# Kernel optimization log

Hardware: AMD Instinct MI355X
Metric: run time of the kernel (lower is better)

Reference implementation:

```python
import jax, jax.numpy as jnp
import numpy as np

B, S, H, NH = 2, 2048, 2048, 16
HD = H // NH  # 128


def setup_inputs() -> dict:
    key = jax.random.key(0)
    ks = jax.random.split(key, 10)
    scale = 0.02
    hidden_states = jax.random.normal(ks[0], (B, S, H), dtype=jnp.float32)
    # additive causal mask [1,1,S,S]
    causal = jnp.tril(jnp.ones((S, S), dtype=jnp.bool_))
    attention_mask = jnp.where(causal, 0.0, -1e9).astype(jnp.float32)[None, None]
    def lin(k):
        kw, kb = jax.random.split(k)
        return (jax.random.normal(kw, (H, H), dtype=jnp.float32) * scale,
                jnp.zeros((H,), dtype=jnp.float32))
    Wq, bq = lin(ks[1])
    Wk, bk = lin(ks[2])
    Wv, bv = lin(ks[3])
    Wo, bo = lin(ks[4])
    return {"hidden_states": hidden_states, "attention_mask": attention_mask,
            "Wq": Wq, "bq": bq, "Wk": Wk, "bk": bk, "Wv": Wv, "bv": bv,
            "Wo": Wo, "bo": bo}


def reference(hidden_states, attention_mask, Wq, bq, Wk, bk, Wv, bv, Wo, bo):
    b, s, h = hidden_states.shape
    def shape(t):  # [b,s,h] -> [b,nh,s,hd]
        return t.reshape(b, s, NH, HD).transpose(0, 2, 1, 3)
    q = shape(hidden_states @ Wq.T + bq)
    k = shape(hidden_states @ Wk.T + bk)
    v = shape(hidden_states @ Wv.T + bv)
    attn = jnp.einsum('bnqd,bnkd->bnqk', q, k) / jnp.sqrt(jnp.float32(HD))
    attn = attn + attention_mask
    attn = jax.nn.softmax(attn, axis=-1)
    out = jnp.einsum('bnqk,bnkd->bnqd', attn, v)
    out = out.transpose(0, 2, 1, 3).reshape(b, s, h)
    return out @ Wo.T + bo
```

## Files before the change

kernel.cpp:

```cpp
#include <hip/hip_runtime.h>
#include <hip/hip_bf16.h>

#define SEQ   2048
#define HDIM  2048
#define NHEAD 16
#define HEADD 128
#define BATCH 2
#define MTOT  (BATCH*SEQ)
#define BH    (BATCH*NHEAD)

typedef __attribute__((ext_vector_type(8))) __bf16 bf16x8;
typedef __attribute__((ext_vector_type(4))) float f32x4;
typedef __attribute__((ext_vector_type(16))) float f32x16;
typedef __attribute__((ext_vector_type(8))) unsigned short u16x8;

__device__ __forceinline__ unsigned short f2b(float f) {
    __bf16 h = (__bf16)f;
    return __builtin_bit_cast(unsigned short, h);
}

__device__ __forceinline__ void gld_lds16(const void* gptr, void* ldsptr) {
    __builtin_amdgcn_global_load_lds(
        (const __attribute__((address_space(1))) unsigned int*)gptr,
        (__attribute__((address_space(3))) unsigned int*)ldsptr,
        16, 0, 0);
}

__global__ void cvt_bf16(const float* __restrict__ src, unsigned short* __restrict__ dst, long n8) {
    long i = blockIdx.x * (long)blockDim.x + threadIdx.x;
    long stride = (long)gridDim.x * blockDim.x;
    for (; i < n8; i += stride) {
        f32x4 a = *(const f32x4*)(src + i * 8);
        f32x4 b = *(const f32x4*)(src + i * 8 + 4);
        u16x8 o;
#pragma unroll
        for (int j = 0; j < 4; ++j) { o[j] = f2b(a[j]); o[4 + j] = f2b(b[j]); }
        *(u16x8*)(dst + i * 8) = o;
    }
}

__global__ void cvt5(const float* __restrict__ s0, const float* __restrict__ s1,
                     const float* __restrict__ s2, const float* __restrict__ s3,
                     const float* __restrict__ s4,
                     unsigned short* __restrict__ d0, unsigned short* __restrict__ d1,
                     unsigned short* __restrict__ d2, unsigned short* __restrict__ d3,
                     unsigned short* __restrict__ d4,
                     long n0, long n1) {
    const float* s; unsigned short* d; long n;
    switch (blockIdx.z) {
        case 0: s = s0; d = d0; n = n0; break;
        case 1: s = s1; d = d1; n = n1; break;
        case 2: s = s2; d = d2; n = n1; break;
        case 3: s = s3; d = d3; n = n1; break;
        default: s = s4; d = d4; n = n1; break;
    }
    long i = blockIdx.x * (long)blockDim.x + threadIdx.x;
    long stride = (long)gridDim.x * blockDim.x;
    for (; i < n; i += stride) {
        f32x4 a = *(const f32x4*)(s + i * 8);
        f32x4 b = *(const f32x4*)(s + i * 8 + 4);
        u16x8 o;
#pragma unroll
        for (int j = 0; j < 4; ++j) { o[j] = f2b(a[j]); o[4 + j] = f2b(b[j]); }
        *(u16x8*)(d + i * 8) = o;
    }
}

__launch_bounds__(256)
__global__ void gemm_qkv(const unsigned short* __restrict__ A,
                         const unsigned short* __restrict__ Bw,
                         const float* __restrict__ bq, const float* __restrict__ bk,
                         const float* __restrict__ bv,
                         unsigned short* __restrict__ Cout, float rs) {
    __shared__ unsigned short As[128 * 32];
    __shared__ unsigned short Bs[128 * 32];
    const int tid  = threadIdx.x;
    const int lane = tid & 63;
    const int w    = tid >> 6;

    const int wgid = blockIdx.y * gridDim.x + blockIdx.x;
    const int cpx  = (gridDim.x * gridDim.y) >> 3;
    const int swz  = (wgid & 7) * cpx + (wgid >> 3);
    const int m0  = (swz % gridDim.x) * 128;
    const int n0g = (swz / gridDim.x) * 128;

    const int wr = (w >> 1) * 64, wc = (w & 1) * 64;
    const long rowBytes = (long)HDIM * 2;

    const char* Ab = (const char*)A  + (long)m0  * rowBytes;
    const char* Bb = (const char*)Bw + (long)n0g * rowBytes;

    f32x4 acc[4][4] = {};

    const int kIters = HDIM >> 5;
    for (int kt = 0; kt < kIters; ++kt) {
        const long kb = (long)kt * 64;
#pragma unroll
        for (int i = 0; i < 2; ++i) {
            int c = tid + i * 256;
            int row = c >> 2;
            int cb  = (c & 3) * 16;
            gld_lds16(Ab + (long)row * rowBytes + kb + cb, (char*)As + c * 16);
            gld_lds16(Bb + (long)row * rowBytes + kb + cb, (char*)Bs + c * 16);
        }
        __syncthreads();
        bf16x8 af[4], bfr[4];
#pragma unroll
        for (int f = 0; f < 4; ++f) {
            af[f]  = *(const bf16x8*)&As[(wr + f * 16 + (lane & 15)) * 32 + (lane >> 4) * 8];
            bfr[f] = *(const bf16x8*)&Bs[(wc + f * 16 + (lane & 15)) * 32 + (lane >> 4) * 8];
        }
#pragma unroll
        for (int mf = 0; mf < 4; ++mf)
#pragma unroll
            for (int nf = 0; nf < 4; ++nf)
                acc[mf][nf] = __builtin_amdgcn_mfma_f32_16x16x32_bf16(af[mf], bfr[nf], acc[mf][nf], 0, 0, 0);
        __syncthreads();
    }

    const int mat = n0g >> 11;
    const float* bb = (mat == 0) ? bq : (mat == 1) ? bk : bv;
    const float scale = (mat == 0) ? rs : 1.0f;
    unsigned short* O = Cout + (long)mat * 8388608;

#pragma unroll
    for (int mf = 0; mf < 4; ++mf) {
#pragma unroll
        for (int nf = 0; nf < 4; ++nf) {
            int nn = (n0g + wc + nf * 16 + (lane & 15)) & 2047;
            int nh = nn >> 7, hd = nn & 127;
            float bv_ = bb[nn];
#pragma unroll
            for (int j = 0; j < 4; ++j) {
                int m = m0 + wr + mf * 16 + (lane >> 4) * 4 + j;
                int b = m >> 11, s = m & 2047;
                float v = (acc[mf][nf][j] + bv_) * scale;
                long idx;
                if (mat < 2) idx = ((long)(b * NHEAD + nh) * SEQ + s) * HEADD + hd;
                else         idx = ((long)(b * NHEAD + nh) * HEADD + hd) * SEQ + s;
                O[idx] = f2b(v);
            }
        }
    }
}

__launch_bounds__(256)
__global__ void gemm_out(const unsigned short* __restrict__ A,
                         const unsigned short* __restrict__ Bw,
                         const float* __restrict__ bias,
                         float* __restrict__ Cout) {
    __shared__ unsigned short As[128 * 32];
    __shared__ unsigned short Bs[128 * 32];
    const int tid  = threadIdx.x;
    const int lane = tid & 63;
    const int w    = tid >> 6;

    const int wgid = blockIdx.y * gridDim.x + blockIdx.x;
    const int cpx  = (gridDim.x * gridDim.y) >> 3;
    const int swz  = (wgid & 7) * cpx + (wgid >> 3);
    const int m0 = (swz % gridDim.x) * 128, n0 = (swz / gridDim.x) * 128;

    const int wr = (w >> 1) * 64, wc = (w & 1) * 64;
    const long rowBytes = (long)HDIM * 2;

    f32x4 acc[4][4] = {};

    const int kIters = HDIM >> 5;
    for (int kt = 0; kt < kIters; ++kt) {
        const long kb = (long)kt * 64;
#pragma unroll
        for (int i = 0; i < 2; ++i) {
            int c = tid + i * 256;
            int row = c >> 2;
            int cb  = (c & 3) * 16;
            gld_lds16((const char*)A  + (long)(m0 + row) * rowBytes + kb + cb, (char*)As + c * 16);
            gld_lds16((const char*)Bw + (long)(n0 + row) * rowBytes + kb + cb, (char*)Bs + c * 16);
        }
        __syncthreads();
        bf16x8 af[4], bfr[4];
#pragma unroll
        for (int f = 0; f < 4; ++f) {
            af[f]  = *(const bf16x8*)&As[(wr + f * 16 + (lane & 15)) * 32 + (lane >> 4) * 8];
            bfr[f] = *(const bf16x8*)&Bs[(wc + f * 16 + (lane & 15)) * 32 + (lane >> 4) * 8];
        }
#pragma unroll
        for (int mf = 0; mf < 4; ++mf)
#pragma unroll
            for (int nf = 0; nf < 4; ++nf)
                acc[mf][nf] = __builtin_amdgcn_mfma_f32_16x16x32_bf16(af[mf], bfr[nf], acc[mf][nf], 0, 0, 0);
        __syncthreads();
    }

#pragma unroll
    for (int mf = 0; mf < 4; ++mf) {
#pragma unroll
        for (int nf = 0; nf < 4; ++nf) {
            int n = n0 + wc + nf * 16 + (lane & 15);
            float bv = bias[n];
#pragma unroll
            for (int j = 0; j < 4; ++j) {
                int m = m0 + wr + mf * 16 + (lane >> 4) * 4 + j;
                Cout[(long)m * HDIM + n] = acc[mf][nf][j] + bv;
            }
        }
    }
}

#define MASKV (-3.0e38f)

__device__ __forceinline__ void attn_step32s(
    const unsigned short* Ksb, const unsigned short* Vsb,
    const bf16x8 (&qf)[8], f32x16 (&acc)[4], float& mrun, float& lrun,
    int lane, int p, int q0w, int kvt, bool diag)
{
    const int ql = lane & 31;
    const int hi = lane >> 5;

    f32x16 sv = {};
    {
        const int row = p * 32 + ql;
        const int sw  = (row & 7) << 4;
        __builtin_amdgcn_s_setprio(1);
#pragma unroll
        for (int kc = 0; kc < 8; ++kc) {
            int off = (row * 256 + ((kc * 32 + hi * 16) ^ sw)) >> 1;
            bf16x8 kf = *(const bf16x8*)&Ksb[off];
            sv = __builtin_amdgcn_mfma_f32_32x32x16_bf16(kf, qf[kc], sv, 0, 0, 0);
        }
        __builtin_amdgcn_s_setprio(0);
    }

    if (diag) {
        const int qg = q0w + ql;
#pragma unroll
        for (int r = 0; r < 16; ++r) {
            int kv = kvt * 64 + p * 32 + (r & 3) + 8 * (r >> 2) + 4 * hi;
            if (kv > qg) sv[r] = MASKV;
        }
    }

    float tmax = sv[0];
#pragma unroll
    for (int r = 1; r < 16; ++r) tmax = fmaxf(tmax, sv[r]);
    tmax = fmaxf(tmax, __shfl_xor(tmax, 32));

    float mnew = mrun, sc = 1.0f;
    if (__any(tmax > mrun + 11.5f)) {
        mnew = fmaxf(mrun, tmax);
        sc = exp2f(mrun - mnew);
#pragma unroll
        for (int db = 0; db < 4; ++db) acc[db] *= sc;
    }
    float rsum = 0.f;
#pragma unroll
    for (int r = 0; r < 16; ++r) {
        float pv = exp2f(sv[r] - mnew);
        sv[r] = pv;
        rsum += pv;
    }
    rsum += __shfl_xor(rsum, 32);
    lrun = lrun * sc + rsum;
    mrun = mnew;

    bf16x8 pf[2];
#pragma unroll
    for (int kc2 = 0; kc2 < 2; ++kc2) {
        unsigned int w01 = f2b(sv[8 * kc2 + 0]) | ((unsigned int)f2b(sv[8 * kc2 + 1]) << 16);
        unsigned int w23 = f2b(sv[8 * kc2 + 2]) | ((unsigned int)f2b(sv[8 * kc2 + 3]) << 16);
        unsigned int w45 = f2b(sv[8 * kc2 + 4]) | ((unsigned int)f2b(sv[8 * kc2 + 5]) << 16);
        unsigned int w67 = f2b(sv[8 * kc2 + 6]) | ((unsigned int)f2b(sv[8 * kc2 + 7]) << 16);
        asm volatile("v_permlane32_swap_b32 %0, %1" : "+v"(w01), "+v"(w45));
        asm volatile("v_permlane32_swap_b32 %0, %1" : "+v"(w23), "+v"(w67));
        union { unsigned int u[4]; bf16x8 v; } pk;
        pk.u[0] = w01; pk.u[1] = w23; pk.u[2] = w45; pk.u[3] = w67;
        pf[kc2] = pk.v;
    }

    __builtin_amdgcn_s_setprio(1);
#pragma unroll
    for (int db = 0; db < 4; ++db) {
        const int row = db * 32 + ql;
        const int sw  = (row & 7) << 4;
#pragma unroll
        for (int kc2 = 0; kc2 < 2; ++kc2) {
            int off = (row * 128 + ((p * 64 + kc2 * 32 + hi * 16) ^ sw)) >> 1;
            bf16x8 vf = *(const bf16x8*)&Vsb[off];
            acc[db] = __builtin_amdgcn_mfma_f32_32x32x16_bf16(vf, pf[kc2], acc[db], 0, 0, 0);
        }
    }
    __builtin_amdgcn_s_setprio(0);
}

__device__ __forceinline__ void attn_merge_store(
    f32x16 (&acc)[4], float mrun, float lrun,
    float (*Mx)[32], float (*Lx)[32], f32x16 (*Ob)[64],
    unsigned short* __restrict__ Out, long rowbase, int lane, int wp, int p)
{
    const int ql = lane & 31, hi = lane >> 5;
    Mx[wp * 2 + p][ql] = mrun;
    Lx[wp * 2 + p][ql] = lrun;
    __syncthreads();
    const float mo = Mx[wp * 2 + 1 - p][ql];
    const float lo = Lx[wp * 2 + 1 - p][ql];
    const float M  = fmaxf(mrun, mo);
    const float a  = exp2f(mrun - M);
    const float L  = lrun * a + lo * exp2f(mo - M);
#pragma unroll
    for (int db = 0; db < 4; ++db) acc[db] *= a;
#pragma unroll
    for (int db = 0; db < 4; ++db) {
        if (p == 1) Ob[wp][lane] = acc[db];
        __syncthreads();
        if (p == 0) acc[db] += Ob[wp][lane];
        __syncthreads();
    }
    if (p == 0) {
        const float inv = 1.0f / L;
        const long base = rowbase + (long)ql * HDIM;
#pragma unroll
        for (int db = 0; db < 4; ++db)
#pragma unroll
            for (int mm = 0; mm < 4; ++mm) {
                int d0 = db * 32 + 8 * mm + 4 * hi;
                unsigned int w0 = f2b(acc[db][4 * mm + 0] * inv) | ((unsigned int)f2b(acc[db][4 * mm + 1] * inv) << 16);
                unsigned int w1 = f2b(acc[db][4 * mm + 2] * inv) | ((unsigned int)f2b(acc[db][4 * mm + 3] * inv) << 16);
                *(unsigned long long*)(Out + base + d0) =
                    (unsigned long long)w0 | ((unsigned long long)w1 << 32);
            }
    }
}

__launch_bounds__(512, 1)
__global__ void attn_fwd(const unsigned short* __restrict__ Q,
                         const unsigned short* __restrict__ K,
                         const unsigned short* __restrict__ Vt,
                         unsigned short* __restrict__ Out) {
    __shared__ unsigned short Ks[2][64 * 128];
    __shared__ unsigned short Vs[2][128 * 64];
    __shared__ float Mx[8][32];
    __shared__ float Lx[8][32];
    __shared__ f32x16 Ob[4][64];

    const int tid  = threadIdx.x;
    const int lane = tid & 63;
    const int w    = tid >> 6;
    const int wp   = w & 3;
    const int p    = w >> 2;

    const int id  = blockIdx.x;
    const int xcd = id & 7;
    const int j   = id >> 3;
    const int bh  = xcd * 4 + (j >> 3);
    const int x   = j & 7;
    const int hiT = 15 - x;
    const int loT = x;
    const int nA  = 2 * hiT + 2;
    const int nB  = 2 * loT + 2;
    const int q0A = hiT * 128 + wp * 32;
    const int q0B = loT * 128 + wp * 32;

    const char* Kbase = (const char*)(K  + (long)bh * SEQ * HEADD);
    const char* Vbase = (const char*)(Vt + (long)bh * HEADD * SEQ);

#define STAGE(kvt, bb) do {                                                             \
    _Pragma("unroll")                                                                   \
    for (int i = 0; i < 2; ++i) {                                                       \
        int c = tid + i * 512;                                                          \
        int rowk = c >> 4;                                                              \
        int cbk  = ((c & 15) * 16) ^ ((rowk & 7) << 4);                                 \
        gld_lds16(Kbase + (long)((kvt) * 64 + rowk) * 256 + cbk, (char*)Ks[bb] + c * 16);\
        int rowv = c >> 3;                                                              \
        int cbv  = ((c & 7) * 16) ^ ((rowv & 7) << 4);                                  \
        gld_lds16(Vbase + (long)rowv * (SEQ * 2) + (kvt) * 128 + cbv, (char*)Vs[bb] + c * 16); \
    } } while (0)

    const int b = bh >> 4, nh = bh & 15;
    int buf = 0;

    STAGE(0, 0);
    __syncthreads();

    {
        bf16x8 qf[8];
#pragma unroll
        for (int kc = 0; kc < 8; ++kc)
            qf[kc] = *(const bf16x8*)&Q[((long)bh * SEQ + q0A + (lane & 31)) * HEADD + kc * 16 + (lane >> 5) * 8];

        f32x16 acc[4] = {};
        float mrun = -1e30f, lrun = 0.f;
        for (int s = 0; s < nA; ++s) {
            if (s + 1 < nA) STAGE(s + 1, buf ^ 1);
            else            STAGE(0, buf ^ 1);
            attn_step32s(Ks[buf], Vs[buf], qf, acc, mrun, lrun,
                         lane, p, q0A, s, s * 64 + 63 > q0A);
            __syncthreads();
            buf ^= 1;
        }
        attn_merge_store(acc, mrun, lrun, Mx, Lx, Ob, Out,
                         ((long)(b * SEQ) + q0A) * HDIM + nh * HEADD, lane, wp, p);
    }

    {
        bf16x8 qf[8];
#pragma unroll
        for (int kc = 0; kc < 8; ++kc)
            qf[kc] = *(const bf16x8*)&Q[((long)bh * SEQ + q0B + (lane & 31)) * HEADD + kc * 16 + (lane >> 5) * 8];

        f32x16 acc[4] = {};
        float mrun = -1e30f, lrun = 0.f;
        for (int s = 0; s < nB; ++s) {
            if (s + 1 < nB) STAGE(s + 1, buf ^ 1);
            attn_step32s(Ks[buf], Vs[buf], qf, acc, mrun, lrun,
                         lane, p, q0B, s, s * 64 + 63 > q0B);
            __syncthreads();
            buf ^= 1;
        }
        attn_merge_store(acc, mrun, lrun, Mx, Lx, Ob, Out,
                         ((long)(b * SEQ) + q0B) * HDIM + nh * HEADD, lane, wp, p);
    }
#undef STAGE
}

extern "C" void kernel_launch(void* const* d_in, const int* in_sizes, int n_in,
                              void* d_out, int out_size, void* d_ws, size_t ws_size,
                              hipStream_t stream) {
    const float* hs = (const float*)d_in[0];
    const float* Wq = (const float*)d_in[2];
    const float* bq = (const float*)d_in[3];
    const float* Wk = (const float*)d_in[4];
    const float* bk = (const float*)d_in[5];
    const float* Wv = (const float*)d_in[6];
    const float* bv = (const float*)d_in[7];
    const float* Wo = (const float*)d_in[8];
    const float* bo = (const float*)d_in[9];
    float* out = (float*)d_out;

    char* ws = (char*)d_ws;
    const long MB = 1024L * 1024L;
    const float rs = 0.08838834764831845f * 1.4426950408889634f;

    if (ws_size >= 96 * MB) {
        unsigned short* hsb  = (unsigned short*)ws;
        unsigned short* wqkv = (unsigned short*)(ws + 16 * MB);
        unsigned short* wob  = (unsigned short*)(ws + 40 * MB);
        unsigned short* qb   = (unsigned short*)(ws + 48 * MB);
        unsigned short* kb   = (unsigned short*)(ws + 64 * MB);
        unsigned short* vtb  = (unsigned short*)(ws + 80 * MB);
        unsigned short* aob  = hsb;
        unsigned short* wqb  = wqkv;
        unsigned short* wkb  = wqkv + 2048L * 2048;
        unsigned short* wvb  = wqkv + 2L * 2048 * 2048;

        cvt5<<<dim3(1024, 1, 5), 256, 0, stream>>>(
            hs, Wq, Wk, Wv, Wo,
            hsb, wqb, wkb, wvb, wob,
            (long)MTOT * HDIM / 8, (long)HDIM * HDIM / 8);
        gemm_qkv<<<dim3(32, 48), 256, 0, stream>>>(hsb, wqkv, bq, bk, bv, qb, rs);
        attn_fwd<<<256, 512, 0, stream>>>(qb, kb, vtb, aob);
        gemm_out<<<dim3(32, 16), 256, 0, stream>>>(aob, wob, bo, out);
    } else {
        unsigned short* hsb = (unsigned short*)ws;
        unsigned short* wb  = (unsigned short*)(ws + 16 * MB);
        unsigned short* qb  = (unsigned short*)(ws + 40 * MB);
        unsigned short* kb  = (unsigned short*)(ws + 56 * MB);
        unsigned short* vtb = (unsigned short*)(ws + 72 * MB);
        unsigned short* aob = hsb;

        cvt_bf16<<<2048, 256, 0, stream>>>(hs, hsb, (long)MTOT * HDIM / 8);
        cvt_bf16<<<2048, 256, 0, stream>>>(Wq, wb, (long)HDIM * HDIM / 8);
        cvt_bf16<<<2048, 256, 0, stream>>>(Wk, wb + 2048L * 2048, (long)HDIM * HDIM / 8);
        cvt_bf16<<<2048, 256, 0, stream>>>(Wv, wb + 2L * 2048 * 2048, (long)HDIM * HDIM / 8);
        gemm_qkv<<<dim3(32, 48), 256, 0, stream>>>(hsb, wb, bq, bk, bv, qb, rs);
        attn_fwd<<<256, 512, 0, stream>>>(qb, kb, vtb, aob);
        cvt_bf16<<<2048, 256, 0, stream>>>(Wo, wb, (long)HDIM * HDIM / 8);
        gemm_out<<<dim3(32, 16), 256, 0, stream>>>(aob, wb == 0 ? (const unsigned short*)0 : wb, bo, out);
    }
}
```

Measured before the change: 295.8 us.

## Triple-buffer GEMM K-loop with async LDS loads and transpose V stores via LDS

Merges the QKV and output projection GEMMs into one templated kernel whose K-loop uses a three-stage LDS ring buffer. Tiles are prefetched two steps ahead and waited on with vmcnt counters, with a single barrier per iteration and raised wave priority around the MFMA block. This is meant to hide global-load latency that the old load, sync, compute, sync loop exposed. The V output, which is stored transposed, is now staged through LDS so each thread writes contiguous 16-byte vectors instead of scattered 2-byte stores. The cost is 48 KB of LDS per block, which may reduce occupancy.

```diff
diff --git a/kernel.cpp b/kernel.cpp
--- a/kernel.cpp
+++ b/kernel.cpp
@@ -66,14 +66,14 @@
     }
 }
 
+template <int MODE>
 __launch_bounds__(256)
-__global__ void gemm_qkv(const unsigned short* __restrict__ A,
-                         const unsigned short* __restrict__ Bw,
-                         const float* __restrict__ bq, const float* __restrict__ bk,
-                         const float* __restrict__ bv,
-                         unsigned short* __restrict__ Cout, float rs) {
-    __shared__ unsigned short As[128 * 32];
-    __shared__ unsigned short Bs[128 * 32];
+__global__ void gemm_p(const unsigned short* __restrict__ A,
+                       const unsigned short* __restrict__ Bw,
+                       const float* __restrict__ b0, const float* __restrict__ b1,
+                       const float* __restrict__ b2,
+                       void* __restrict__ Cout, float rs) {
+    __shared__ char LDS[49152];
     const int tid  = threadIdx.x;
     const int lane = tid & 63;
     const int w    = tid >> 6;
@@ -85,122 +85,120 @@
     const int n0g = (swz / gridDim.x) * 128;
 
     const int wr = (w >> 1) * 64, wc = (w & 1) * 64;
-    const long rowBytes = (long)HDIM * 2;
-
-    const char* Ab = (const char*)A  + (long)m0  * rowBytes;
-    const char* Bb = (const char*)Bw + (long)n0g * rowBytes;
+    const long rowB = (long)HDIM * 2;
+
+    const char* Ab = (const char*)A  + (long)m0  * rowB;
+    const char* Bb = (const char*)Bw + (long)n0g * rowB;
+
+#define STG(T, bi) do {                                                          \
+    _Pragma("unroll")                                                            \
+    for (int i_ = 0; i_ < 2; ++i_) {                                             \
+        int c = tid + i_ * 256; int row = c >> 2; int cb = (c & 3) * 16;         \
+        gld_lds16(Ab + (long)row * rowB + (T) * 64 + cb,                         \
+                  LDS + (bi) * 8192 + c * 16);                                   \
+        gld_lds16(Bb + (long)row * rowB + (T) * 64 + cb,                         \
+                  LDS + 24576 + (bi) * 8192 + c * 16);                           \
+    } } while (0)
 
     f32x4 acc[4][4] = {};
-
-    const int kIters = HDIM >> 5;
-    for (int kt = 0; kt < kIters; ++kt) {
-        const long kb = (long)kt * 64;
-#pragma unroll
-        for (int i = 0; i < 2; ++i) {
-            int c = tid + i * 256;
-            int row = c >> 2;
-            int cb  = (c & 3) * 16;
-            gld_lds16(Ab + (long)row * rowBytes + kb + cb, (char*)As + c * 16);
-            gld_lds16(Bb + (long)row * rowBytes + kb + cb, (char*)Bs + c * 16);
-        }
-        __syncthreads();
+    const int NT = HDIM / 32;
+
+    STG(0, 0);
+    STG(1, 1);
+    asm volatile("s_waitcnt vmcnt(4)" ::: "memory");
+    __builtin_amdgcn_s_barrier();
+
+    int bi = 0;
+    for (int t = 0; t < NT; ++t) {
+        if (t + 2 < NT) {
+            int nb = bi + 2; if (nb >= 3) nb -= 3;
+            STG(t + 2, nb);
+        }
+        const char* Ar = LDS + bi * 8192;
+        const char* Br = LDS + 24576 + bi * 8192;
         bf16x8 af[4], bfr[4];
 #pragma unroll
         for (int f = 0; f < 4; ++f) {
-            af[f]  = *(const bf16x8*)&As[(wr + f * 16 + (lane & 15)) * 32 + (lane >> 4) * 8];
-            bfr[f] = *(const bf16x8*)&Bs[(wc + f * 16 + (lane & 15)) * 32 + (lane >> 4) * 8];
-        }
+            af[f]  = *(const bf16x8*)(Ar + (wr + f * 16 + (lane & 15)) * 64 + (lane >> 4) * 16);
+            bfr[f] = *(const bf16x8*)(Br + (wc + f * 16 + (lane & 15)) * 64 + (lane >> 4) * 16);
+        }
+        if (t + 2 < NT) asm volatile("s_waitcnt vmcnt(4)" ::: "memory");
+        else            asm volatile("s_waitcnt vmcnt(0)" ::: "memory");
+        __builtin_amdgcn_s_setprio(1);
 #pragma unroll
         for (int mf = 0; mf < 4; ++mf)
 #pragma unroll
             for (int nf = 0; nf < 4; ++nf)
                 acc[mf][nf] = __builtin_amdgcn_mfma_f32_16x16x32_bf16(af[mf], bfr[nf], acc[mf][nf], 0, 0, 0);
-        __syncthreads();
-    }
-
-    const int mat = n0g >> 11;
-    const float* bb = (mat == 0) ? bq : (mat == 1) ? bk : bv;
-    const float scale = (mat == 0) ? rs : 1.0f;
-    unsigned short* O = Cout + (long)mat * 8388608;
-
-#pragma unroll
-    for (int mf = 0; mf < 4; ++mf) {
-#pragma unroll
-        for (int nf = 0; nf < 4; ++nf) {
-            int nn = (n0g + wc + nf * 16 + (lane & 15)) & 2047;
-            int nh = nn >> 7, hd = nn & 127;
-            float bv_ = bb[nn];
-#pragma unroll
-            for (int j = 0; j < 4; ++j) {
-                int m = m0 + wr + mf * 16 + (lane >> 4) * 4 + j;
-                int b = m >> 11, s = m & 2047;
-                float v = (acc[mf][nf][j] + bv_) * scale;
-                long idx;
-                if (mat < 2) idx = ((long)(b * NHEAD + nh) * SEQ + s) * HEADD + hd;
-                else         idx = ((long)(b * NHEAD + nh) * HEADD + hd) * SEQ + s;
-                O[idx] = f2b(v);
+        __builtin_amdgcn_s_setprio(0);
+        __builtin_amdgcn_s_barrier();
+        bi = (bi + 1 >= 3) ? 0 : bi + 1;
+    }
+#undef STG
+
+    if (MODE == 0) {
+        const int mat = n0g >> 11;
+        const float* bb = (mat == 0) ? b0 : (mat == 1) ? b1 : b2;
+        unsigned short* O = (unsigned short*)Cout + (long)mat * 8388608;
+        if (mat < 2) {
+            const float scale = (mat == 0) ? rs : 1.0f;
+#pragma unroll
+            for (int mf = 0; mf < 4; ++mf) {
+#pragma unroll
+                for (int nf = 0; nf < 4; ++nf) {
+                    int nn = (n0g + wc + nf * 16 + (lane & 15)) & 2047;
+                    int nh = nn >> 7, hd = nn & 127;
+                    float bv_ = bb[nn];
+#pragma unroll
+                    for (int j = 0; j < 4; ++j) {
+                        int m = m0 + wr + mf * 16 + (lane >> 4) * 4 + j;
+                        int b = m >> 11, s = m & 2047;
+                        float v = (acc[mf][nf][j] + bv_) * scale;
+                        O[((long)(b * NHEAD + nh) * SEQ + s) * HEADD + hd] = f2b(v);
+                    }
+                }
             }
-        }
-    }
-}
-
-__launch_bounds__(256)
-__global__ void gemm_out(const unsigned short* __restrict__ A,
-                         const unsigned short* __restrict__ Bw,
-                         const float* __restrict__ bias,
-                         float* __restrict__ Cout) {
-    __shared__ unsigned short As[128 * 32];
-    __shared__ unsigned short Bs[128 * 32];
-    const int tid  = threadIdx.x;
-    const int lane = tid & 63;
-    const int w    = tid >> 6;
-
-    const int wgid = blockIdx.y * gridDim.x + blockIdx.x;
-    const int cpx  = (gridDim.x * gridDim.y) >> 3;
-    const int swz  = (wgid & 7) * cpx + (wgid >> 3);
-    const int m0 = (swz % gridDim.x) * 128, n0 = (swz / gridDim.x) * 128;
-
-    const int wr = (w >> 1) * 64, wc = (w & 1) * 64;
-    const long rowBytes = (long)HDIM * 2;
-
-    f32x4 acc[4][4] = {};
-
-    const int kIters = HDIM >> 5;
-    for (int kt = 0; kt < kIters; ++kt) {
-        const long kb = (long)kt * 64;
-#pragma unroll
-        for (int i = 0; i < 2; ++i) {
-            int c = tid + i * 256;
-            int row = c >> 2;
-            int cb  = (c & 3) * 16;
-            gld_lds16((const char*)A  + (long)(m0 + row) * rowBytes + kb + cb, (char*)As + c * 16);
-            gld_lds16((const char*)Bw + (long)(n0 + row) * rowBytes + kb + cb, (char*)Bs + c * 16);
-        }
-        __syncthreads();
-        bf16x8 af[4], bfr[4];
-#pragma unroll
-        for (int f = 0; f < 4; ++f) {
-            af[f]  = *(const bf16x8*)&As[(wr + f * 16 + (lane & 15)) * 32 + (lane >> 4) * 8];
-            bfr[f] = *(const bf16x8*)&Bs[(wc + f * 16 + (lane & 15)) * 32 + (lane >> 4) * 8];
-        }
-#pragma unroll
-        for (int mf = 0; mf < 4; ++mf)
-#pragma unroll
-            for (int nf = 0; nf < 4; ++nf)
-                acc[mf][nf] = __builtin_amdgcn_mfma_f32_16x16x32_bf16(af[mf], bfr[nf], acc[mf][nf], 0, 0, 0);
-        __syncthreads();
-    }
-
-#pragma unroll
-    for (int mf = 0; mf < 4; ++mf) {
-#pragma unroll
-        for (int nf = 0; nf < 4; ++nf) {
-            int n = n0 + wc + nf * 16 + (lane & 15);
-            float bv = bias[n];
-#pragma unroll
-            for (int j = 0; j < 4; ++j) {
-                int m = m0 + wr + mf * 16 + (lane >> 4) * 4 + j;
-                Cout[(long)m * HDIM + n] = acc[mf][nf][j] + bv;
+        } else {
+            unsigned short* Tr = (unsigned short*)LDS;
+            const int nn0 = n0g & 2047;
+#pragma unroll
+            for (int mf = 0; mf < 4; ++mf) {
+#pragma unroll
+                for (int nf = 0; nf < 4; ++nf) {
+                    int nl = wc + nf * 16 + (lane & 15);
+                    float bv_ = bb[nn0 + nl];
+#pragma unroll
+                    for (int j = 0; j < 4; j += 2) {
+                        int ml = wr + mf * 16 + (lane >> 4) * 4 + j;
+                        unsigned int pk = f2b(acc[mf][nf][j] + bv_)
+                                        | ((unsigned int)f2b(acc[mf][nf][j + 1] + bv_) << 16);
+                        *(unsigned int*)((char*)Tr + nl * 272 + ml * 2) = pk;
+                    }
+                }
+            }
+            __syncthreads();
+            const int nh  = nn0 >> 7;
+            const int row = tid >> 1, half = tid & 1;
+            const int b = m0 >> 11, s0 = m0 & 2047;
+            unsigned short* dst = O + ((long)(b * NHEAD + nh) * HEADD + row) * SEQ + s0 + half * 64;
+            const unsigned short* srcl = Tr + row * 136 + half * 64;
+#pragma unroll
+            for (int k = 0; k < 8; ++k)
+                *(u16x8*)(dst + k * 8) = *(const u16x8*)(srcl + k * 8);
+        }
+    } else {
+        float* O = (float*)Cout;
+#pragma unroll
+        for (int mf = 0; mf < 4; ++mf) {
+#pragma unroll
+            for (int nf = 0; nf < 4; ++nf) {
+                int n = n0g + wc + nf * 16 + (lane & 15);
+                float bv = b0[n];
+#pragma unroll
+                for (int j = 0; j < 4; ++j) {
+                    int m = m0 + wr + mf * 16 + (lane >> 4) * 4 + j;
+                    O[(long)m * HDIM + n] = acc[mf][nf][j] + bv;
+                }
             }
         }
     }
@@ -455,24 +453,24 @@
             hs, Wq, Wk, Wv, Wo,
             hsb, wqb, wkb, wvb, wob,
             (long)MTOT * HDIM / 8, (long)HDIM * HDIM / 8);
-        gemm_qkv<<<dim3(32, 48), 256, 0, stream>>>(hsb, wqkv, bq, bk, bv, qb, rs);
+        gemm_p<0><<<dim3(32, 48), 256, 0, stream>>>(hsb, wqkv, bq, bk, bv, qb, rs);
         attn_fwd<<<256, 512, 0, stream>>>(qb, kb, vtb, aob);
-        gemm_out<<<dim3(32, 16), 256, 0, stream>>>(aob, wob, bo, out);
+        gemm_p<2><<<dim3(32, 16), 256, 0, stream>>>(aob, wob, bo, bo, bo, out, 1.0f);
     } else {
-        unsigned short* hsb = (unsigned short*)ws;
-        unsigned short* wb  = (unsigned short*)(ws + 16 * MB);
-        unsigned short* qb  = (unsigned short*)(ws + 40 * MB);
-        unsigned short* kb  = (unsigned short*)(ws + 56 * MB);
-        unsigned short* vtb = (unsigned short*)(ws + 72 * MB);
-        unsigned short* aob = hsb;
+        unsigned short* hsb  = (unsigned short*)ws;
+        unsigned short* wqkv = (unsigned short*)(ws + 16 * MB);
+        unsigned short* qb   = (unsigned short*)(ws + 40 * MB);
+        unsigned short* kb   = (unsigned short*)(ws + 56 * MB);
+        unsigned short* vtb  = (unsigned short*)(ws + 72 * MB);
+        unsigned short* aob  = hsb;
 
         cvt_bf16<<<2048, 256, 0, stream>>>(hs, hsb, (long)MTOT * HDIM / 8);
-        cvt_bf16<<<2048, 256, 0, stream>>>(Wq, wb, (long)HDIM * HDIM / 8);
-        cvt_bf16<<<2048, 256, 0, stream>>>(Wk, wb + 2048L * 2048, (long)HDIM * HDIM / 8);
-        cvt_bf16<<<2048, 256, 0, stream>>>(Wv, wb + 2L * 2048 * 2048, (long)HDIM * HDIM / 8);
-        gemm_qkv<<<dim3(32, 48), 256, 0, stream>>>(hsb, wb, bq, bk, bv, qb, rs);
+        cvt_bf16<<<2048, 256, 0, stream>>>(Wq, wqkv, (long)HDIM * HDIM / 8);
+        cvt_bf16<<<2048, 256, 0, stream>>>(Wk, wqkv + 2048L * 2048, (long)HDIM * HDIM / 8);
+        cvt_bf16<<<2048, 256, 0, stream>>>(Wv, wqkv + 2L * 2048 * 2048, (long)HDIM * HDIM / 8);
+        gemm_p<0><<<dim3(32, 48), 256, 0, stream>>>(hsb, wqkv, bq, bk, bv, qb, rs);
         attn_fwd<<<256, 512, 0, stream>>>(qb, kb, vtb, aob);
-        cvt_bf16<<<2048, 256, 0, stream>>>(Wo, wb, (long)HDIM * HDIM / 8);
-        gemm_out<<<dim3(32, 16), 256, 0, stream>>>(aob, wb == 0 ? (const unsigned short*)0 : wb, bo, out);
-    }
-}
+        cvt_bf16<<<2048, 256, 0, stream>>>(Wo, wqkv, (long)HDIM * HDIM / 8);
+        gemm_p<2><<<dim3(32, 16), 256, 0, stream>>>(aob, wqkv, bo, bo, bo, out, 1.0f);
+    }
+}
```

New measurement: 277.4 us. -6.2%, faster.
